# Optimization experiments

Measured on AMD Instinct MI355X. Metric: run time of the kernel, lower is better.

## Reference

```python
import jax, jax.numpy as jnp
import numpy as np
import math

H = 8
D_MODEL = 512
SEQ = 1024  # afr_reduced_cnn_size -> becomes sequence/channel axis
B = 16
KSIZE = 7
D_K = D_MODEL // H


def setup_inputs() -> dict:
    key = jax.random.key(0)
    ks = jax.random.split(key, 9)
    s = 0.02
    return {
        "query": jax.random.normal(ks[0], (B, SEQ, D_MODEL), jnp.float32),
        "key": jax.random.normal(ks[1], (B, SEQ, D_MODEL), jnp.float32),
        "value": jax.random.normal(ks[2], (B, SEQ, D_MODEL), jnp.float32),
        # causal conv params for K and V projections (convs[1], convs[2]); convs[0] is unused in forward
        "conv_k_w": jax.random.normal(ks[3], (SEQ, SEQ, KSIZE), jnp.float32) * s,
        "conv_k_b": jnp.zeros((SEQ,), jnp.float32),
        "conv_v_w": jax.random.normal(ks[4], (SEQ, SEQ, KSIZE), jnp.float32) * s,
        "conv_v_b": jnp.zeros((SEQ,), jnp.float32),
        # output linear (torch Linear: weight [out, in])
        "lin_w": jax.random.normal(ks[5], (D_MODEL, D_MODEL), jnp.float32) * s,
        "lin_b": jnp.zeros((D_MODEL,), jnp.float32),
    }


def _causal_conv1d(x, w, b):
    # x: [B, C, L]; w: [O, I, K]; left-pad K-1 for causality
    pad = w.shape[-1] - 1
    y = jax.lax.conv_general_dilated(
        x, w, window_strides=(1,), padding=[(pad, 0)],
        dimension_numbers=("NCH", "OIH", "NCH"))
    return y + b[None, :, None]


def reference(query, key, value, conv_k_w, conv_k_b, conv_v_w, conv_v_b, lin_w, lin_b):
    nb = query.shape[0]
    # [B, S, d_model] -> [B, h, N, d_k]
    q = query.reshape(nb, -1, H, D_K).transpose(0, 2, 1, 3)
    k = _causal_conv1d(key, conv_k_w, conv_k_b).reshape(nb, -1, H, D_K).transpose(0, 2, 1, 3)
    v = _causal_conv1d(value, conv_v_w, conv_v_b).reshape(nb, -1, H, D_K).transpose(0, 2, 1, 3)
    scores = jnp.einsum("bhnd,bhmd->bhnm", q, k) / math.sqrt(D_K)
    p_attn = jax.nn.softmax(scores, axis=-1)  # dropout is identity at eval
    x = jnp.einsum("bhnm,bhmd->bhnd", p_attn, v)
    x = x.transpose(0, 2, 1, 3).reshape(nb, -1, H * D_K)
    return x @ lin_w.T + lin_b
```

## Files before the change

kernel.cpp:

```cpp
#include <hip/hip_runtime.h>
#include <hip/hip_bf16.h>

typedef unsigned short u16;
typedef __attribute__((ext_vector_type(8))) __bf16 bf16x8;
typedef __attribute__((ext_vector_type(4))) float f32x4;
typedef __attribute__((ext_vector_type(4))) unsigned short u16x4;

#define DEVI static __device__ __forceinline__

DEVI u16 f2bf(float f) {
    union { float f; unsigned u; } v; v.f = f;
    unsigned r = v.u + 0x7fffu + ((v.u >> 16) & 1u);
    return (u16)(r >> 16);
}

DEVI unsigned cvt_pk_bf16(float lo, float hi) {
    unsigned r;
    asm("v_cvt_pk_bf16_f32 %0, %1, %2" : "=v"(r) : "v"(lo), "v"(hi));
    return r;
}

DEVI void gload16(const u16* g, u16* l) {
    __builtin_amdgcn_global_load_lds(
        (const __attribute__((address_space(1))) void*)g,
        (__attribute__((address_space(3))) void*)l, 16, 0, 0);
}


__global__ void k_cast_scale(const float* __restrict__ src, u16* __restrict__ dst,
                             int n, float scale) {
    int i = (blockIdx.x * blockDim.x + threadIdx.x) * 4;
    if (i >= n) return;
    float4 v = *(const float4*)(src + i);
    u16x4 o = { f2bf(v.x * scale), f2bf(v.y * scale), f2bf(v.z * scale), f2bf(v.w * scale) };
    *(u16x4*)(dst + i) = o;
}

__global__ void k_castW(const float* __restrict__ w, u16* __restrict__ wt) {
    int oi = blockIdx.x * blockDim.x + threadIdx.x;
    const float* p = w + (size_t)oi * 7;
#pragma unroll
    for (int t = 0; t < 7; ++t)
        wt[(size_t)t * 1048576 + oi] = f2bf(p[t]);
}

__global__ void k_transpose_pad(const float* __restrict__ x, u16* __restrict__ out) {
    __shared__ float tile[64][65];
    int b = blockIdx.z;
    int l0 = blockIdx.x * 64, i0 = blockIdx.y * 64;
    int t = threadIdx.x;
    const float* xb = x + (size_t)b * 1024 * 512;
    u16* ob = out + (size_t)b * 520 * 1024;
    int tr = t >> 4, tc = (t & 15) * 4;
#pragma unroll
    for (int r = 0; r < 4; ++r) {
        int row = tr + r * 16;
        float4 v = *(const float4*)(xb + (size_t)(i0 + row) * 512 + l0 + tc);
        tile[row][tc + 0] = v.x; tile[row][tc + 1] = v.y;
        tile[row][tc + 2] = v.z; tile[row][tc + 3] = v.w;
    }
    __syncthreads();
#pragma unroll
    for (int r = 0; r < 4; ++r) {
        int lr = tr + r * 16;
        u16x4 o = { f2bf(tile[tc + 0][lr]), f2bf(tile[tc + 1][lr]),
                    f2bf(tile[tc + 2][lr]), f2bf(tile[tc + 3][lr]) };
        *(u16x4*)(ob + (size_t)(l0 + 6 + lr) * 1024 + i0 + tc) = o;
    }
}

__global__ __launch_bounds__(512, 2)
void k_conv256(const u16* __restrict__ WtK, const u16* __restrict__ WtV,
               const u16* __restrict__ XtK, const u16* __restrict__ XtV,
               const float* __restrict__ bK, const float* __restrict__ bV,
               u16* __restrict__ YK, u16* __restrict__ YV) {
    __shared__ __align__(16) u16 As[2][16384];
    __shared__ __align__(16) u16 Bs[2][16896];
    int id = blockIdx.x;
    int xcd = id & 7, inner = id >> 3;
    bool isV = xcd & 1;
    int o0 = (xcd >> 1) * 256;
    int b = inner & 15;
    int l0 = (inner >> 4) * 256;
    const u16* Wt = isV ? WtV : WtK;
    const u16* Xb = (isV ? XtV : XtK) + (size_t)b * 520 * 1024;
    int tid = threadIdx.x, lane = tid & 63, wave = tid >> 6;
    int q = lane & 15, g = lane >> 4;
    int wm = wave >> 2, wn = wave & 3;

    int sr = tid >> 3;
    int ss = (tid & 7) ^ (sr & 7);

    auto stageA = [&](int ic, int t, int slot) {
        const u16* a = Wt + ((size_t)t << 20) + (size_t)(o0 + sr) * 1024 + (ic << 6) + ss * 8;
        u16* ad = &As[slot][tid * 8];
#pragma unroll
        for (int l = 0; l < 4; ++l)
            gload16(a + (size_t)(l << 6) * 1024, ad + (l << 12));
    };
    auto stageB = [&](int ic, int slot) {
        const u16* bb = Xb + (size_t)(l0 + sr) * 1024 + (ic << 6) + ss * 8;
        u16* bd = &Bs[slot][tid * 8];
#pragma unroll
        for (int l = 0; l < 4; ++l)
            gload16(bb + (size_t)(l << 6) * 1024, bd + (l << 12));
        int sr5 = 256 + ((tid >> 3) & 7);
        gload16(Xb + (size_t)(l0 + sr5) * 1024 + (ic << 6) + ss * 8,
                &Bs[slot][sr5 * 64 + (tid & 7) * 8]);
    };

    f32x4 acc[8][4] = {};

    stageB(0, 0);
    stageA(0, 0, 0);
    stageA(0, 1, 1);
    asm volatile("s_waitcnt vmcnt(4)" ::: "memory");
    __builtin_amdgcn_s_barrier();

    int ic2 = 0, t2 = 2;
    for (int ic = 0; ic < 16; ++ic) {
        int bslot = ic & 1;
        const u16* Bsl = Bs[bslot];
        for (int t = 0; t < 7; ++t) {
            int s = ic * 7 + t;
            const u16* Asl = As[s & 1];
            bf16x8 bfr[4][2], af[4][2];
#pragma unroll
            for (int nf = 0; nf < 4; ++nf) {
                int r = wn * 64 + nf * 16 + q + t;
                const u16* base = Bsl + r * 64;
#pragma unroll
                for (int kk = 0; kk < 2; ++kk)
                    bfr[nf][kk] = *(const bf16x8*)(base + (((kk * 4 + g) ^ (r & 7)) << 3));
            }
#pragma unroll
            for (int mf = 0; mf < 4; ++mf) {
                int r = wm * 128 + mf * 16 + q;
                const u16* base = Asl + r * 64;
#pragma unroll
                for (int kk = 0; kk < 2; ++kk)
                    af[mf][kk] = *(const bf16x8*)(base + (((kk * 4 + g) ^ (r & 7)) << 3));
            }
            __builtin_amdgcn_s_setprio(1);
#pragma unroll
            for (int mf = 0; mf < 4; ++mf)
#pragma unroll
                for (int nf = 0; nf < 4; ++nf)
#pragma unroll
                    for (int kk = 0; kk < 2; ++kk)
                        acc[mf][nf] = __builtin_amdgcn_mfma_f32_16x16x32_bf16(
                            af[mf][kk], bfr[nf][kk], acc[mf][nf], 0, 0, 0);
            __builtin_amdgcn_s_setprio(0);
#pragma unroll
            for (int mf = 0; mf < 4; ++mf) {
                int r = wm * 128 + 64 + mf * 16 + q;
                const u16* base = Asl + r * 64;
#pragma unroll
                for (int kk = 0; kk < 2; ++kk)
                    af[mf][kk] = *(const bf16x8*)(base + (((kk * 4 + g) ^ (r & 7)) << 3));
            }
            __builtin_amdgcn_s_setprio(1);
#pragma unroll
            for (int mf = 0; mf < 4; ++mf)
#pragma unroll
                for (int nf = 0; nf < 4; ++nf)
#pragma unroll
                    for (int kk = 0; kk < 2; ++kk)
                        acc[4 + mf][nf] = __builtin_amdgcn_mfma_f32_16x16x32_bf16(
                            af[mf][kk], bfr[nf][kk], acc[4 + mf][nf], 0, 0, 0);
            __builtin_amdgcn_s_setprio(0);

            asm volatile("" ::: "memory");
            __builtin_amdgcn_s_barrier();
            bool haveB = (t == 2) && (ic < 15);
            if (s + 2 < 112) {
                stageA(ic2, t2, s & 1);
                if (++t2 == 7) { t2 = 0; ++ic2; }
                if (haveB) stageB(ic + 1, bslot ^ 1);
                if (haveB || (t == 3 && ic < 15))
                    asm volatile("s_waitcnt vmcnt(9)" ::: "memory");
                else
                    asm volatile("s_waitcnt vmcnt(4)" ::: "memory");
            } else {
                asm volatile("s_waitcnt vmcnt(0)" ::: "memory");
            }
            __builtin_amdgcn_s_barrier();
        }
    }

    const float* bias = isV ? bV : bK;
#pragma unroll
    for (int mf = 0; mf < 8; ++mf) {
        int ro = o0 + wm * 128 + mf * 16 + g * 4;
        float b0 = bias[ro + 0], b1 = bias[ro + 1], b2 = bias[ro + 2], b3 = bias[ro + 3];
#pragma unroll
        for (int nf = 0; nf < 4; ++nf) {
            int co = l0 + wn * 64 + nf * 16 + q;
            f32x4 a = acc[mf][nf];
            if (isV) {
                u16x4 o = { f2bf(a[0] + b0), f2bf(a[1] + b1), f2bf(a[2] + b2), f2bf(a[3] + b3) };
                *(u16x4*)&YV[((size_t)b * 512 + co) * 1024 + ro] = o;
            } else {
                u16* yp = &YK[((size_t)b * 1024 + ro) * 512 + co];
                yp[0]    = f2bf(a[0] + b0);
                yp[512]  = f2bf(a[1] + b1);
                yp[1024] = f2bf(a[2] + b2);
                yp[1536] = f2bf(a[3] + b3);
            }
        }
    }
}

__global__ __launch_bounds__(512, 4)
void k_attn2(const u16* __restrict__ Q, const u16* __restrict__ K,
             const u16* __restrict__ Vt, u16* __restrict__ O) {
    __shared__ __align__(16) u16 Ks[2][64 * 64];
    __shared__ __align__(16) u16 Vs[2][64 * 64];
    int b = blockIdx.z, h = blockIdx.y, q0 = blockIdx.x * 128;
    int tid = threadIdx.x, lane = tid & 63, wave = tid >> 6;
    int g = lane >> 4, q = lane & 15;

    const u16* Kb = K + (size_t)b * 1024 * 512 + h * 64;
    const u16* Vb = Vt + ((size_t)b * 512 + h * 64) * 1024;
    const u16* Qb = Q + ((size_t)b * 1024 + q0 + wave * 16 + q) * 512 + h * 64;

    bf16x8 qf[2];
    qf[0] = *(const bf16x8*)(Qb + g * 8);
    qf[1] = *(const bf16x8*)(Qb + 32 + g * 8);

    int sr = tid >> 3;
    int ss = (tid & 7) ^ (sr & 7);
    const u16* ksrc = Kb + (size_t)sr * 512 + ss * 8;
    const u16* vsrc = Vb + (size_t)sr * 1024 + ss * 8;

    f32x4 o[4] = {};
    float lsum = 0.f;

    gload16(ksrc, &Ks[0][tid * 8]);
    gload16(vsrc, &Vs[0][tid * 8]);
    __syncthreads();

#pragma unroll 2
    for (int t = 0; t < 16; ++t) {
        int buf = t & 1;
        if (t < 15) {
            gload16(ksrc + (size_t)(t + 1) * 64 * 512, &Ks[buf ^ 1][tid * 8]);
            gload16(vsrc + (t + 1) * 64, &Vs[buf ^ 1][tid * 8]);
        }
        f32x4 s[4];
#pragma unroll
        for (int mf = 0; mf < 4; ++mf) {
            int r = 16 * mf + q;
            const u16* base = &Ks[buf][r * 64];
            bf16x8 kf0 = *(const bf16x8*)(base + (((g) ^ (q & 7)) << 3));
            bf16x8 kf1 = *(const bf16x8*)(base + (((4 + g) ^ (q & 7)) << 3));
            f32x4 zz = {};
            zz = __builtin_amdgcn_mfma_f32_16x16x32_bf16(kf0, qf[0], zz, 0, 0, 0);
            s[mf] = __builtin_amdgcn_mfma_f32_16x16x32_bf16(kf1, qf[1], zz, 0, 0, 0);
        }
        unsigned w[4][2];
#pragma unroll
        for (int mf = 0; mf < 4; ++mf) {
            f32x4 p;
#pragma unroll
            for (int j = 0; j < 4; ++j) {
                p[j] = exp2f(s[mf][j]);
                lsum += p[j];
            }
            w[mf][0] = cvt_pk_bf16(p[0], p[1]);
            w[mf][1] = cvt_pk_bf16(p[2], p[3]);
        }
        bool hi = lane >= 32;
        int ia = ((g & 1) << 5) + q;
        int ib = ia + 16;
#pragma unroll
        for (int c = 0; c < 2; ++c) {
            unsigned a0 = __shfl(w[2 * c][0], ia), b0 = __shfl(w[2 * c + 1][0], ia);
            unsigned a1 = __shfl(w[2 * c][1], ia), b1 = __shfl(w[2 * c + 1][1], ia);
            unsigned a2 = __shfl(w[2 * c][0], ib), b2 = __shfl(w[2 * c + 1][0], ib);
            unsigned a3 = __shfl(w[2 * c][1], ib), b3 = __shfl(w[2 * c + 1][1], ib);
            union { unsigned u[4]; bf16x8 v8; } pu;
            pu.u[0] = hi ? b0 : a0;
            pu.u[1] = hi ? b1 : a1;
            pu.u[2] = hi ? b2 : a2;
            pu.u[3] = hi ? b3 : a3;
            bf16x8 pb = pu.v8;
#pragma unroll
            for (int df = 0; df < 4; ++df) {
                int rd = 16 * df + q;
                bf16x8 vf = *(const bf16x8*)(&Vs[buf][rd * 64] + (((c * 4 + g) ^ (q & 7)) << 3));
                o[df] = __builtin_amdgcn_mfma_f32_16x16x32_bf16(vf, pb, o[df], 0, 0, 0);
            }
        }
        __syncthreads();
    }

    lsum += __shfl_xor(lsum, 16);
    lsum += __shfl_xor(lsum, 32);
    float inv = 1.0f / lsum;

    unsigned wo[4][2];
#pragma unroll
    for (int df = 0; df < 4; ++df) {
        f32x4 v = o[df];
        v[0] *= inv; v[1] *= inv; v[2] *= inv; v[3] *= inv;
        wo[df][0] = cvt_pk_bf16(v[0], v[1]);
        wo[df][1] = cvt_pk_bf16(v[2], v[3]);
    }
    bool hi = lane >= 32;
    int ia = ((g & 1) << 5) + q;
    int ib = ia + 16;
    u16* Ob = O + ((size_t)b * 1024 + q0 + wave * 16 + q) * 512 + h * 64;
#pragma unroll
    for (int c = 0; c < 2; ++c) {
        unsigned a0 = __shfl(wo[2 * c][0], ia), b0 = __shfl(wo[2 * c + 1][0], ia);
        unsigned a1 = __shfl(wo[2 * c][1], ia), b1 = __shfl(wo[2 * c + 1][1], ia);
        unsigned a2 = __shfl(wo[2 * c][0], ib), b2 = __shfl(wo[2 * c + 1][0], ib);
        unsigned a3 = __shfl(wo[2 * c][1], ib), b3 = __shfl(wo[2 * c + 1][1], ib);
        int4 st;
        st.x = (int)(hi ? b0 : a0);
        st.y = (int)(hi ? b1 : a1);
        st.z = (int)(hi ? b2 : a2);
        st.w = (int)(hi ? b3 : a3);
        *(int4*)(Ob + c * 32 + g * 8) = st;
    }
}

__global__ __launch_bounds__(256, 2)
void k_gemm_out(const u16* __restrict__ A, const u16* __restrict__ Bt,
                const float* __restrict__ bias, float* __restrict__ C) {
    __shared__ __align__(16) u16 As[128 * 64];
    __shared__ __align__(16) u16 Bs[128 * 64];
    int n0 = blockIdx.x * 128, m0 = blockIdx.y * 128;
    int tid = threadIdx.x, lane = tid & 63, wave = tid >> 6;
    int wr = (wave >> 1) * 64, wc = (wave & 1) * 64;
    f32x4 acc[4][4] = {};

    for (int kk = 0; kk < 8; ++kk) {
        int i0 = kk * 64;
        const u16* asrc = A + (size_t)(m0 + (tid >> 3)) * 512 + i0 + (tid & 7) * 8;
        const u16* bsrc = Bt + (size_t)(n0 + (tid >> 3)) * 512 + i0 + (tid & 7) * 8;
        __syncthreads();
#pragma unroll
        for (int s = 0; s < 4; ++s) {
            gload16(asrc + (size_t)s * 32 * 512, &As[s * 2048 + tid * 8]);
            gload16(bsrc + (size_t)s * 32 * 512, &Bs[s * 2048 + tid * 8]);
        }
        __syncthreads();
#pragma unroll
        for (int ks = 0; ks < 2; ++ks) {
            bf16x8 af[4], bfr[4];
#pragma unroll
            for (int m = 0; m < 4; ++m)
                af[m] = *(const bf16x8*)&As[(wr + m * 16 + (lane & 15)) * 64 + ks * 32 + (lane >> 4) * 8];
#pragma unroll
            for (int n = 0; n < 4; ++n)
                bfr[n] = *(const bf16x8*)&Bs[(wc + n * 16 + (lane & 15)) * 64 + ks * 32 + (lane >> 4) * 8];
#pragma unroll
            for (int m = 0; m < 4; ++m)
#pragma unroll
                for (int n = 0; n < 4; ++n)
                    acc[m][n] = __builtin_amdgcn_mfma_f32_16x16x32_bf16(af[m], bfr[n], acc[m][n], 0, 0, 0);
        }
    }

#pragma unroll
    for (int m = 0; m < 4; ++m) {
        int ro = m0 + wr + m * 16 + (lane >> 4) * 4;
#pragma unroll
        for (int n = 0; n < 4; ++n) {
            int co = n0 + wc + n * 16 + (lane & 15);
            float bb = bias[co];
            float* cp = &C[(size_t)ro * 512 + co];
            cp[0]    = acc[m][n][0] + bb;
            cp[512]  = acc[m][n][1] + bb;
            cp[1024] = acc[m][n][2] + bb;
            cp[1536] = acc[m][n][3] + bb;
        }
    }
}

extern "C" void kernel_launch(void* const* d_in, const int* in_sizes, int n_in,
                              void* d_out, int out_size, void* d_ws, size_t ws_size,
                              hipStream_t stream) {
    (void)in_sizes; (void)n_in; (void)out_size; (void)ws_size;
    const float* query = (const float*)d_in[0];
    const float* key   = (const float*)d_in[1];
    const float* value = (const float*)d_in[2];
    const float* wk    = (const float*)d_in[3];
    const float* bk    = (const float*)d_in[4];
    const float* wv    = (const float*)d_in[5];
    const float* bv    = (const float*)d_in[6];
    const float* lw    = (const float*)d_in[7];
    const float* lb    = (const float*)d_in[8];
    float* out = (float*)d_out;

    u16* ws16  = (u16*)d_ws;
    u16* q_bf  = ws16;
    u16* k_att = q_bf  + 8388608;
    u16* v_t   = k_att + 8388608;
    u16* x_att = v_t   + 8388608;
    u16* xt_k  = x_att + 8388608;
    u16* xt_v  = xt_k  + 8519680;
    u16* wk_bf = xt_v  + 8519680;
    u16* wv_bf = wk_bf + 7340032;
    u16* lw_bf = wv_bf + 7340032;

    hipMemsetAsync(xt_k, 0, (size_t)2 * 8519680 * sizeof(u16), stream);

    k_cast_scale<<<8192, 256, 0, stream>>>(query, q_bf, 8388608, 0.125f * 1.44269504f);
    k_cast_scale<<<256, 256, 0, stream>>>(lw, lw_bf, 262144, 1.0f);
    k_castW<<<4096, 256, 0, stream>>>(wk, wk_bf);
    k_castW<<<4096, 256, 0, stream>>>(wv, wv_bf);
    k_transpose_pad<<<dim3(8, 16, 16), 256, 0, stream>>>(key, xt_k);
    k_transpose_pad<<<dim3(8, 16, 16), 256, 0, stream>>>(value, xt_v);

    k_conv256<<<dim3(256, 1, 1), 512, 0, stream>>>(wk_bf, wv_bf, xt_k, xt_v, bk, bv, k_att, v_t);

    k_attn2<<<dim3(8, 8, 16), 512, 0, stream>>>(q_bf, k_att, v_t, x_att);

    k_gemm_out<<<dim3(4, 128), 256, 0, stream>>>(x_att, lw_bf, lb, out);
}
```

Baseline: 338.9 us.

## Split conv GEMM inner step into four barrier-separated MFMA phases

```diff
diff --git a/kernel.cpp b/kernel.cpp
--- a/kernel.cpp
+++ b/kernel.cpp
@@ -124,15 +124,8 @@
         for (int t = 0; t < 7; ++t) {
             int s = ic * 7 + t;
             const u16* Asl = As[s & 1];
-            bf16x8 bfr[4][2], af[4][2];
-#pragma unroll
-            for (int nf = 0; nf < 4; ++nf) {
-                int r = wn * 64 + nf * 16 + q + t;
-                const u16* base = Bsl + r * 64;
-#pragma unroll
-                for (int kk = 0; kk < 2; ++kk)
-                    bfr[nf][kk] = *(const bf16x8*)(base + (((kk * 4 + g) ^ (r & 7)) << 3));
-            }
+            bf16x8 af[4][2], bf0[2][2], bf1[2][2];
+
 #pragma unroll
             for (int mf = 0; mf < 4; ++mf) {
                 int r = wm * 128 + mf * 16 + q;
@@ -141,16 +134,48 @@
                 for (int kk = 0; kk < 2; ++kk)
                     af[mf][kk] = *(const bf16x8*)(base + (((kk * 4 + g) ^ (r & 7)) << 3));
             }
+#pragma unroll
+            for (int nf = 0; nf < 2; ++nf) {
+                int r = wn * 64 + nf * 16 + q + t;
+                const u16* base = Bsl + r * 64;
+#pragma unroll
+                for (int kk = 0; kk < 2; ++kk)
+                    bf0[nf][kk] = *(const bf16x8*)(base + (((kk * 4 + g) ^ (r & 7)) << 3));
+            }
+            __builtin_amdgcn_s_barrier();
             __builtin_amdgcn_s_setprio(1);
 #pragma unroll
             for (int mf = 0; mf < 4; ++mf)
 #pragma unroll
-                for (int nf = 0; nf < 4; ++nf)
+                for (int nf = 0; nf < 2; ++nf)
 #pragma unroll
                     for (int kk = 0; kk < 2; ++kk)
                         acc[mf][nf] = __builtin_amdgcn_mfma_f32_16x16x32_bf16(
-                            af[mf][kk], bfr[nf][kk], acc[mf][nf], 0, 0, 0);
+                            af[mf][kk], bf0[nf][kk], acc[mf][nf], 0, 0, 0);
             __builtin_amdgcn_s_setprio(0);
+            __builtin_amdgcn_s_barrier();
+
+#pragma unroll
+            for (int nf = 0; nf < 2; ++nf) {
+                int r = wn * 64 + (2 + nf) * 16 + q + t;
+                const u16* base = Bsl + r * 64;
+#pragma unroll
+                for (int kk = 0; kk < 2; ++kk)
+                    bf1[nf][kk] = *(const bf16x8*)(base + (((kk * 4 + g) ^ (r & 7)) << 3));
+            }
+            __builtin_amdgcn_s_barrier();
+            __builtin_amdgcn_s_setprio(1);
+#pragma unroll
+            for (int mf = 0; mf < 4; ++mf)
+#pragma unroll
+                for (int nf = 0; nf < 2; ++nf)
+#pragma unroll
+                    for (int kk = 0; kk < 2; ++kk)
+                        acc[mf][2 + nf] = __builtin_amdgcn_mfma_f32_16x16x32_bf16(
+                            af[mf][kk], bf1[nf][kk], acc[mf][2 + nf], 0, 0, 0);
+            __builtin_amdgcn_s_setprio(0);
+            __builtin_amdgcn_s_barrier();
+
 #pragma unroll
             for (int mf = 0; mf < 4; ++mf) {
                 int r = wm * 128 + 64 + mf * 16 + q;
@@ -159,24 +184,39 @@
                 for (int kk = 0; kk < 2; ++kk)
                     af[mf][kk] = *(const bf16x8*)(base + (((kk * 4 + g) ^ (r & 7)) << 3));
             }
+            __builtin_amdgcn_s_barrier();
             __builtin_amdgcn_s_setprio(1);
 #pragma unroll
             for (int mf = 0; mf < 4; ++mf)
 #pragma unroll
-                for (int nf = 0; nf < 4; ++nf)
+                for (int nf = 0; nf < 2; ++nf)
 #pragma unroll
                     for (int kk = 0; kk < 2; ++kk)
                         acc[4 + mf][nf] = __builtin_amdgcn_mfma_f32_16x16x32_bf16(
-                            af[mf][kk], bfr[nf][kk], acc[4 + mf][nf], 0, 0, 0);
+                            af[mf][kk], bf0[nf][kk], acc[4 + mf][nf], 0, 0, 0);
             __builtin_amdgcn_s_setprio(0);
-
-            asm volatile("" ::: "memory");
-            __builtin_amdgcn_s_barrier();
+            __builtin_amdgcn_s_barrier();
+
             bool haveB = (t == 2) && (ic < 15);
             if (s + 2 < 112) {
                 stageA(ic2, t2, s & 1);
                 if (++t2 == 7) { t2 = 0; ++ic2; }
                 if (haveB) stageB(ic + 1, bslot ^ 1);
+            }
+            __builtin_amdgcn_s_barrier();
+            __builtin_amdgcn_s_setprio(1);
+#pragma unroll
+            for (int mf = 0; mf < 4; ++mf)
+#pragma unroll
+                for (int nf = 0; nf < 2; ++nf)
+#pragma unroll
+                    for (int kk = 0; kk < 2; ++kk)
+                        acc[4 + mf][2 + nf] = __builtin_amdgcn_mfma_f32_16x16x32_bf16(
+                            af[mf][kk], bf1[nf][kk], acc[4 + mf][2 + nf], 0, 0, 0);
+            __builtin_amdgcn_s_setprio(0);
+
+            __builtin_amdgcn_s_barrier();
+            if (s + 2 < 112) {
                 if (haveB || (t == 3 && ic < 15))
                     asm volatile("s_waitcnt vmcnt(9)" ::: "memory");
                 else
```

After: 342.1 us. About the same (+0.9%).

## Use 32x32x16 MFMA in causal conv GEMM and zero pad rows in-kernel

Applied to the files above, without the earlier changes.

```diff
diff --git a/kernel.cpp b/kernel.cpp
--- a/kernel.cpp
+++ b/kernel.cpp
@@ -4,6 +4,7 @@
 typedef unsigned short u16;
 typedef __attribute__((ext_vector_type(8))) __bf16 bf16x8;
 typedef __attribute__((ext_vector_type(4))) float f32x4;
+typedef __attribute__((ext_vector_type(16))) float f32x16;
 typedef __attribute__((ext_vector_type(4))) unsigned short u16x4;
 
 #define DEVI static __device__ __forceinline__
@@ -51,6 +52,11 @@
     int t = threadIdx.x;
     const float* xb = x + (size_t)b * 1024 * 512;
     u16* ob = out + (size_t)b * 520 * 1024;
+    if (blockIdx.x == 0 && t < 96) {
+        int pr = t >> 4, pc = (t & 15) * 4;
+        u16x4 z = { 0, 0, 0, 0 };
+        *(u16x4*)(ob + (size_t)pr * 1024 + i0 + pc) = z;
+    }
     int tr = t >> 4, tc = (t & 15) * 4;
 #pragma unroll
     for (int r = 0; r < 4; ++r) {
@@ -85,7 +91,7 @@
     const u16* Wt = isV ? WtV : WtK;
     const u16* Xb = (isV ? XtV : XtK) + (size_t)b * 520 * 1024;
     int tid = threadIdx.x, lane = tid & 63, wave = tid >> 6;
-    int q = lane & 15, g = lane >> 4;
+    int col = lane & 31, hi5 = lane >> 5;
     int wm = wave >> 2, wn = wave & 3;
 
     int sr = tid >> 3;
@@ -109,7 +115,7 @@
                 &Bs[slot][sr5 * 64 + (tid & 7) * 8]);
     };
 
-    f32x4 acc[8][4] = {};
+    f32x16 acc[4][2] = {};
 
     stageB(0, 0);
     stageA(0, 0, 0);
@@ -119,55 +125,62 @@
 
     int ic2 = 0, t2 = 2;
     for (int ic = 0; ic < 16; ++ic) {
-        int bslot = ic & 1;
-        const u16* Bsl = Bs[bslot];
+        const u16* Bsl = Bs[ic & 1];
         for (int t = 0; t < 7; ++t) {
             int s = ic * 7 + t;
             const u16* Asl = As[s & 1];
-            bf16x8 bfr[4][2], af[4][2];
-#pragma unroll
-            for (int nf = 0; nf < 4; ++nf) {
-                int r = wn * 64 + nf * 16 + q + t;
+
+            bf16x8 bfr[2][4];
+#pragma unroll
+            for (int ni = 0; ni < 2; ++ni) {
+                int r = wn * 64 + ni * 32 + col + t;
                 const u16* base = Bsl + r * 64;
 #pragma unroll
-                for (int kk = 0; kk < 2; ++kk)
-                    bfr[nf][kk] = *(const bf16x8*)(base + (((kk * 4 + g) ^ (r & 7)) << 3));
-            }
-#pragma unroll
-            for (int mf = 0; mf < 4; ++mf) {
-                int r = wm * 128 + mf * 16 + q;
+                for (int ks = 0; ks < 4; ++ks) {
+                    int sl = ks * 2 + hi5;
+                    bfr[ni][ks] = *(const bf16x8*)(base + ((sl ^ (r & 7)) << 3));
+                }
+            }
+            bf16x8 af[2][4];
+#pragma unroll
+            for (int mi = 0; mi < 2; ++mi) {
+                int r = wm * 128 + mi * 32 + col;
                 const u16* base = Asl + r * 64;
 #pragma unroll
-                for (int kk = 0; kk < 2; ++kk)
-                    af[mf][kk] = *(const bf16x8*)(base + (((kk * 4 + g) ^ (r & 7)) << 3));
+                for (int ks = 0; ks < 4; ++ks) {
+                    int sl = ks * 2 + hi5;
+                    af[mi][ks] = *(const bf16x8*)(base + ((sl ^ (r & 7)) << 3));
+                }
             }
             __builtin_amdgcn_s_setprio(1);
 #pragma unroll
-            for (int mf = 0; mf < 4; ++mf)
-#pragma unroll
-                for (int nf = 0; nf < 4; ++nf)
-#pragma unroll
-                    for (int kk = 0; kk < 2; ++kk)
-                        acc[mf][nf] = __builtin_amdgcn_mfma_f32_16x16x32_bf16(
-                            af[mf][kk], bfr[nf][kk], acc[mf][nf], 0, 0, 0);
+            for (int mi = 0; mi < 2; ++mi)
+#pragma unroll
+                for (int ni = 0; ni < 2; ++ni)
+#pragma unroll
+                    for (int ks = 0; ks < 4; ++ks)
+                        acc[mi][ni] = __builtin_amdgcn_mfma_f32_32x32x16_bf16(
+                            af[mi][ks], bfr[ni][ks], acc[mi][ni], 0, 0, 0);
             __builtin_amdgcn_s_setprio(0);
 #pragma unroll
-            for (int mf = 0; mf < 4; ++mf) {
-                int r = wm * 128 + 64 + mf * 16 + q;
+            for (int mi = 0; mi < 2; ++mi) {
+                int r = wm * 128 + (2 + mi) * 32 + col;
                 const u16* base = Asl + r * 64;
 #pragma unroll
-                for (int kk = 0; kk < 2; ++kk)
-                    af[mf][kk] = *(const bf16x8*)(base + (((kk * 4 + g) ^ (r & 7)) << 3));
+                for (int ks = 0; ks < 4; ++ks) {
+                    int sl = ks * 2 + hi5;
+                    af[mi][ks] = *(const bf16x8*)(base + ((sl ^ (r & 7)) << 3));
+                }
             }
             __builtin_amdgcn_s_setprio(1);
 #pragma unroll
-            for (int mf = 0; mf < 4; ++mf)
-#pragma unroll
-                for (int nf = 0; nf < 4; ++nf)
-#pragma unroll
-                    for (int kk = 0; kk < 2; ++kk)
-                        acc[4 + mf][nf] = __builtin_amdgcn_mfma_f32_16x16x32_bf16(
-                            af[mf][kk], bfr[nf][kk], acc[4 + mf][nf], 0, 0, 0);
+            for (int mi = 0; mi < 2; ++mi)
+#pragma unroll
+                for (int ni = 0; ni < 2; ++ni)
+#pragma unroll
+                    for (int ks = 0; ks < 4; ++ks)
+                        acc[2 + mi][ni] = __builtin_amdgcn_mfma_f32_32x32x16_bf16(
+                            af[mi][ks], bfr[ni][ks], acc[2 + mi][ni], 0, 0, 0);
             __builtin_amdgcn_s_setprio(0);
 
             asm volatile("" ::: "memory");
@@ -176,7 +189,7 @@
             if (s + 2 < 112) {
                 stageA(ic2, t2, s & 1);
                 if (++t2 == 7) { t2 = 0; ++ic2; }
-                if (haveB) stageB(ic + 1, bslot ^ 1);
+                if (haveB) stageB(ic + 1, (ic & 1) ^ 1);
                 if (haveB || (t == 3 && ic < 15))
                     asm volatile("s_waitcnt vmcnt(9)" ::: "memory");
                 else
@@ -190,22 +203,32 @@
 
     const float* bias = isV ? bV : bK;
 #pragma unroll
-    for (int mf = 0; mf < 8; ++mf) {
-        int ro = o0 + wm * 128 + mf * 16 + g * 4;
-        float b0 = bias[ro + 0], b1 = bias[ro + 1], b2 = bias[ro + 2], b3 = bias[ro + 3];
-#pragma unroll
-        for (int nf = 0; nf < 4; ++nf) {
-            int co = l0 + wn * 64 + nf * 16 + q;
-            f32x4 a = acc[mf][nf];
+    for (int mi = 0; mi < 4; ++mi) {
+#pragma unroll
+        for (int ni = 0; ni < 2; ++ni) {
+            f32x16 a = acc[mi][ni];
+            int co = l0 + wn * 64 + ni * 32 + col;
+            int rb = o0 + wm * 128 + mi * 32 + 4 * hi5;
             if (isV) {
-                u16x4 o = { f2bf(a[0] + b0), f2bf(a[1] + b1), f2bf(a[2] + b2), f2bf(a[3] + b3) };
-                *(u16x4*)&YV[((size_t)b * 512 + co) * 1024 + ro] = o;
+                u16* yp = &YV[((size_t)b * 512 + co) * 1024 + rb];
+#pragma unroll
+                for (int rg = 0; rg < 4; ++rg) {
+                    int ro = rb + 8 * rg;
+                    u16x4 o = { f2bf(a[4 * rg + 0] + bias[ro + 0]),
+                                f2bf(a[4 * rg + 1] + bias[ro + 1]),
+                                f2bf(a[4 * rg + 2] + bias[ro + 2]),
+                                f2bf(a[4 * rg + 3] + bias[ro + 3]) };
+                    *(u16x4*)(yp + 8 * rg) = o;
+                }
             } else {
-                u16* yp = &YK[((size_t)b * 1024 + ro) * 512 + co];
-                yp[0]    = f2bf(a[0] + b0);
-                yp[512]  = f2bf(a[1] + b1);
-                yp[1024] = f2bf(a[2] + b2);
-                yp[1536] = f2bf(a[3] + b3);
+#pragma unroll
+                for (int rg = 0; rg < 4; ++rg) {
+#pragma unroll
+                    for (int j = 0; j < 4; ++j) {
+                        int ro = rb + 8 * rg + j;
+                        YK[((size_t)b * 1024 + ro) * 512 + co] = f2bf(a[4 * rg + j] + bias[ro]);
+                    }
+                }
             }
         }
     }
@@ -406,8 +429,6 @@
     u16* wv_bf = wk_bf + 7340032;
     u16* lw_bf = wv_bf + 7340032;
 
-    hipMemsetAsync(xt_k, 0, (size_t)2 * 8519680 * sizeof(u16), stream);
-
     k_cast_scale<<<8192, 256, 0, stream>>>(query, q_bf, 8388608, 0.125f * 1.44269504f);
     k_cast_scale<<<256, 256, 0, stream>>>(lw, lw_bf, 262144, 1.0f);
     k_castW<<<4096, 256, 0, stream>>>(wk, wk_bf);
```

Result: slower. 347.8 us (+2.6%).
